# Kernel optimization log

Hardware: AMD Instinct MI355X
Metric: run time of the kernel (lower is better)

## Reference

```python
import jax, jax.numpy as jnp
import numpy as np

N_CIRC, N_MIR, N_DIS = 100_000, 50_000, 25_000
IN_CH, HID, OUT = 128, 64, 64


def setup_inputs() -> dict:
    key = jax.random.key(0)
    ks = iter(jax.random.split(key, 64))

    def nrm(shape, scale):
        return jax.random.normal(next(ks), shape, jnp.float32) * scale

    def edges(n_src, n_dst, E):
        s = jax.random.randint(next(ks), (E,), 0, n_src, jnp.int32)
        d = jax.random.randint(next(ks), (E,), 0, n_dst, jnp.int32)
        return jnp.stack([s, d])  # [2, E]

    inp = dict(
        x_circ=nrm((N_CIRC, IN_CH), 1.0),
        x_mir=nrm((N_MIR, IN_CH), 1.0),
        x_dis=nrm((N_DIS, IN_CH), 1.0),
        e_cm=edges(N_CIRC, N_MIR, 500_000),
        e_md=edges(N_MIR, N_DIS, 250_000),
        e_cd=edges(N_CIRC, N_DIS, 250_000),
        e_mc=edges(N_MIR, N_CIRC, 500_000),
        e_dm=edges(N_DIS, N_MIR, 250_000),
        e_dc=edges(N_DIS, N_CIRC, 250_000),
        e_cc=edges(N_CIRC, N_CIRC, 500_000),
        e_mm=edges(N_MIR, N_MIR, 250_000),
        # stacked SAGEConv params: lin_l (with bias) and lin_r (no bias), per relation
        W1l=nrm((6, HID, IN_CH), 0.08), W1r=nrm((6, HID, IN_CH), 0.08), b1=jnp.zeros((6, HID), jnp.float32),
        W2l=nrm((6, HID, HID), 0.12), W2r=nrm((6, HID, HID), 0.12), b2=jnp.zeros((6, HID), jnp.float32),
        W3l=nrm((8, OUT, HID), 0.12), W3r=nrm((8, OUT, HID), 0.12), b3=jnp.zeros((8, OUT), jnp.float32),
    )
    return inp


def _sage(x_src, x_dst, ei, Wl, bl, Wr, n_dst):
    # PyG SAGEConv: out = lin_l(mean_j x_src[j]) + lin_r(x_dst); isolated dst -> 0 agg
    src, dst = ei[0], ei[1]
    msum = jax.ops.segment_sum(x_src[src], dst, num_segments=n_dst)
    cnt = jax.ops.segment_sum(jnp.ones(src.shape, x_src.dtype), dst, num_segments=n_dst)
    agg = msum / jnp.maximum(cnt, 1.0)[:, None]
    return agg @ Wl.T + bl + x_dst @ Wr.T


def _hetero_layer(xc, xm, xd, Wl, Wr, b, es, with_sim):
    e_cm, e_md, e_cd, e_mc, e_dm, e_dc, e_cc, e_mm = es
    o_cm = _sage(xc, xm, e_cm, Wl[0], b[0], Wr[0], N_MIR)
    o_md = _sage(xm, xd, e_md, Wl[1], b[1], Wr[1], N_DIS)
    o_cd = _sage(xc, xd, e_cd, Wl[2], b[2], Wr[2], N_DIS)
    o_mc = _sage(xm, xc, e_mc, Wl[3], b[3], Wr[3], N_CIRC)
    o_dm = _sage(xd, xm, e_dm, Wl[4], b[4], Wr[4], N_MIR)
    o_dc = _sage(xd, xc, e_dc, Wl[5], b[5], Wr[5], N_CIRC)
    if with_sim:
        o_cc = _sage(xc, xc, e_cc, Wl[6], b[6], Wr[6], N_CIRC)
        o_mm = _sage(xm, xm, e_mm, Wl[7], b[7], Wr[7], N_MIR)
        hc = (o_mc + o_dc + o_cc) / 3.0
        hm = (o_cm + o_dm + o_mm) / 3.0
    else:
        hc = (o_mc + o_dc) / 2.0
        hm = (o_cm + o_dm) / 2.0
    hd = (o_md + o_cd) / 2.0  # HeteroConv aggr='mean' across relations
    return hc, hm, hd


def _l2norm(x):
    n = jnp.sqrt(jnp.sum(x * x, axis=1, keepdims=True))
    return x / jnp.maximum(n, 1e-12)


def reference(x_circ, x_mir, x_dis, e_cm, e_md, e_cd, e_mc, e_dm, e_dc, e_cc, e_mm,
              W1l, W1r, b1, W2l, W2r, b2, W3l, W3r, b3):
    es = (e_cm, e_md, e_cd, e_mc, e_dm, e_dc, e_cc, e_mm)
    hc, hm, hd = _hetero_layer(x_circ, x_mir, x_dis, W1l, W1r, b1, es, False)
    hc, hm, hd = jax.nn.relu(hc), jax.nn.relu(hm), jax.nn.relu(hd)  # dropout = identity (eval)
    hc, hm, hd = _hetero_layer(hc, hm, hd, W2l, W2r, b2, es, False)
    hc, hm, hd = jax.nn.relu(hc), jax.nn.relu(hm), jax.nn.relu(hd)
    oc, om, od = _hetero_layer(hc, hm, hd, W3l, W3r, b3, es, True)
    return _l2norm(oc), _l2norm(om), _l2norm(od)
```

## Files before the change

### kernel.cpp

```cpp
#include <hip/hip_runtime.h>
#include <hip/hip_bf16.h>

#define DIV_UP(a,b) (((a)+(b)-1)/(b))

typedef __bf16 bf16x8 __attribute__((ext_vector_type(8)));
typedef float  f32x4  __attribute__((ext_vector_type(4)));

__global__ __launch_bounds__(256) void detect_dtype(const unsigned int* __restrict__ x,
                                                    int* __restrict__ flag) {
  __shared__ int cnt_s;
  if (threadIdx.x == 0) cnt_s = 0;
  __syncthreads();
  unsigned w = x[threadIdx.x];
  unsigned lo_exp = (w >> 7) & 0xFF;
  if (lo_exp >= 100 && lo_exp <= 140) atomicAdd(&cnt_s, 1);
  __syncthreads();
  if (threadIdx.x == 0) flag[0] = (cnt_s >= 128) ? 1 : 0;
}

template<int K>
__global__ __launch_bounds__(256) void gemm_mfma(
    const void* __restrict__ x, int xmode,
    const void* __restrict__ w, int woff, int wmode,
    const int* __restrict__ flagp, __hip_bfloat16* __restrict__ out, int n) {
  constexpr int KP = K + 8;
  __shared__ __bf16 xs[64 * KP];
  const bool xb = (xmode == 2) ? (*flagp != 0) : (xmode == 1);
  const bool wb = (wmode == 2) ? (*flagp != 0) : (wmode == 1);
  const int t = threadIdx.x;
  const int wv = t >> 6;
  const int L = t & 63;
  const int m = L & 15, q = L >> 4;
  const int row0 = blockIdx.x * 64;
  const int col = wv * 16 + m;

  bf16x8 bfr[K / 32];
  if (wb) {
    const __bf16* wh = (const __bf16*)w + woff;
#pragma unroll
    for (int ks = 0; ks < K / 32; ++ks)
      bfr[ks] = *(const bf16x8*)&wh[col * K + ks * 32 + q * 8];
  } else {
    const float* wf = (const float*)w + woff;
#pragma unroll
    for (int ks = 0; ks < K / 32; ++ks) {
      bf16x8 b;
#pragma unroll
      for (int j = 0; j < 8; ++j) b[j] = (__bf16)wf[col * K + ks * 32 + q * 8 + j];
      bfr[ks] = b;
    }
  }

  constexpr int CH = K / 8;
  if (xb) {
    const __bf16* xh = (const __bf16*)x;
    for (int idx = t; idx < 64 * CH; idx += 256) {
      int r = idx / CH, c = idx % CH;
      int gr = row0 + r; gr = (gr < n) ? gr : (n - 1);
      *(bf16x8*)&xs[r * KP + c * 8] = *(const bf16x8*)&xh[(size_t)gr * K + c * 8];
    }
  } else {
    const float* xf = (const float*)x;
    for (int idx = t; idx < 64 * CH; idx += 256) {
      int r = idx / CH, c = idx % CH;
      int gr = row0 + r; gr = (gr < n) ? gr : (n - 1);
      const float* src = &xf[(size_t)gr * K + c * 8];
      bf16x8 v;
#pragma unroll
      for (int j = 0; j < 8; ++j) v[j] = (__bf16)src[j];
      *(bf16x8*)&xs[r * KP + c * 8] = v;
    }
  }
  __syncthreads();

  f32x4 acc[4] = {};
#pragma unroll
  for (int ks = 0; ks < K / 32; ++ks) {
#pragma unroll
    for (int rt = 0; rt < 4; ++rt) {
      bf16x8 a = *(const bf16x8*)&xs[(rt * 16 + m) * KP + ks * 32 + q * 8];
      acc[rt] = __builtin_amdgcn_mfma_f32_16x16x32_bf16(a, bfr[ks], acc[rt], 0, 0, 0);
    }
  }

#pragma unroll
  for (int rt = 0; rt < 4; ++rt) {
#pragma unroll
    for (int i = 0; i < 4; ++i) {
      int gr = row0 + rt * 16 + q * 4 + i;
      if (gr < n) out[(size_t)gr * 64 + col] = __float2bfloat16(acc[rt][i]);
    }
  }
}

template<int K, int MODE>
__global__ __launch_bounds__(256) void fused_agg(
    const void* __restrict__ xdst, int xmode,
    const int* __restrict__ flagp,
    const __hip_bfloat16* __restrict__ wrsum,
    const float* __restrict__ bias,
    const int* __restrict__ col,
    const int* __restrict__ rp0, const __hip_bfloat16* __restrict__ y0,
    const int* __restrict__ rp1, const __hip_bfloat16* __restrict__ y1,
    const int* __restrict__ rp2, const __hip_bfloat16* __restrict__ y2,
    int nrel, float invR,
    void* __restrict__ outp, size_t obase, int n) {
  __shared__ float dbuf[16][68];
  const bool xb = (xmode == 2) ? (*flagp != 0) : (xmode == 1);
  const int t = threadIdx.x;
  const int wv = t >> 6, L = t & 63;
  const int m = L & 15, q = L >> 4;
  const int row0 = blockIdx.x * 16;
  const int colc = wv * 16 + m;

  const __bf16* wh = (const __bf16*)wrsum;
  bf16x8 bfr[K / 32];
#pragma unroll
  for (int ks = 0; ks < K / 32; ++ks)
    bfr[ks] = *(const bf16x8*)&wh[colc * K + ks * 32 + q * 8];

  int ar = row0 + m; ar = (ar < n) ? ar : (n - 1);
  f32x4 acc = {};
  if (xb) {
    const __bf16* xp = (const __bf16*)xdst;
#pragma unroll
    for (int ks = 0; ks < K / 32; ++ks) {
      bf16x8 a = *(const bf16x8*)&xp[(size_t)ar * K + ks * 32 + q * 8];
      acc = __builtin_amdgcn_mfma_f32_16x16x32_bf16(a, bfr[ks], acc, 0, 0, 0);
    }
  } else {
    const float* xp = (const float*)xdst;
#pragma unroll
    for (int ks = 0; ks < K / 32; ++ks) {
      bf16x8 a;
#pragma unroll
      for (int j = 0; j < 8; ++j) a[j] = (__bf16)xp[(size_t)ar * K + ks * 32 + q * 8 + j];
      acc = __builtin_amdgcn_mfma_f32_16x16x32_bf16(a, bfr[ks], acc, 0, 0, 0);
    }
  }
  float bc = bias[colc];
#pragma unroll
  for (int i = 0; i < 4; ++i) dbuf[q * 4 + i][colc] = acc[i] + bc;
  __syncthreads();

  const int* rps[3] = {rp0, rp1, rp2};
  const __hip_bfloat16* ys[3] = {y0, y1, y2};
#pragma unroll 1
  for (int rr = 0; rr < 4; ++rr) {
    int gr = row0 + wv * 4 + rr;
    if (gr >= n) continue;
    float s = dbuf[wv * 4 + rr][L];
#pragma unroll 1
    for (int j = 0; j < nrel; ++j) {
      const int* rp = rps[j];
      const __hip_bfloat16* yy = ys[j];
      int beg = rp[gr], end = rp[gr + 1];
      if (beg == end) continue;
      float g = 0.0f;
      int e = beg;
      for (; e + 4 <= end; e += 4) {
        int c0 = col[e], c1 = col[e + 1], c2 = col[e + 2], c3 = col[e + 3];
        float v0 = __bfloat162float(yy[(size_t)c0 * 64 + L]);
        float v1 = __bfloat162float(yy[(size_t)c1 * 64 + L]);
        float v2 = __bfloat162float(yy[(size_t)c2 * 64 + L]);
        float v3 = __bfloat162float(yy[(size_t)c3 * 64 + L]);
        g += v0 + v1 + v2 + v3;
      }
      for (; e < end; ++e) g += __bfloat162float(yy[(size_t)col[e] * 64 + L]);
      s += g * (1.0f / (float)(end - beg));
    }
    s *= invR;
    if (MODE == 0) {
      ((__hip_bfloat16*)outp)[obase + (size_t)gr * 64 + L] =
          __float2bfloat16(fmaxf(s, 0.0f));
    } else {
      float ss = s * s;
#pragma unroll
      for (int o = 32; o > 0; o >>= 1) ss += __shfl_xor(ss, o, 64);
      float sc = 1.0f / fmaxf(sqrtf(ss), 1e-12f);
      float r = s * sc;
      size_t idx = obase + (size_t)gr * 64 + L;
      if (*flagp) ((__hip_bfloat16*)outp)[idx] = __float2bfloat16(r);
      else        ((float*)outp)[idx] = r;
    }
  }
}

__global__ __launch_bounds__(256) void count_int(const int* __restrict__ ed,
                                                 int* __restrict__ deg, int E) {
  int i = blockIdx.x * 256 + threadIdx.x;
  if (i < E) atomicAdd(&deg[ed[i]], 1);
}

__global__ __launch_bounds__(256) void scan1(const int* __restrict__ deg,
    int* __restrict__ outp, int* __restrict__ part, int n) {
  __shared__ int tmp[256];
  int gid = blockIdx.x * 256 + threadIdx.x;
  int v = (gid < n) ? deg[gid] : 0;
  tmp[threadIdx.x] = v;
  __syncthreads();
  for (int off = 1; off < 256; off <<= 1) {
    int t = (threadIdx.x >= off) ? tmp[threadIdx.x - off] : 0;
    __syncthreads();
    tmp[threadIdx.x] += t;
    __syncthreads();
  }
  if (gid < n) outp[gid] = tmp[threadIdx.x] - v;
  if (threadIdx.x == 255) part[blockIdx.x] = tmp[255];
}

__global__ __launch_bounds__(256) void scan2(int* __restrict__ part, int P,
                                             int* __restrict__ totalout) {
  __shared__ int tmp[256];
  __shared__ int carry;
  if (threadIdx.x == 0) carry = 0;
  __syncthreads();
  for (int base0 = 0; base0 < P; base0 += 256) {
    int i = base0 + threadIdx.x;
    int v = (i < P) ? part[i] : 0;
    tmp[threadIdx.x] = v;
    __syncthreads();
    for (int off = 1; off < 256; off <<= 1) {
      int t = (threadIdx.x >= off) ? tmp[threadIdx.x - off] : 0;
      __syncthreads();
      tmp[threadIdx.x] += t;
      __syncthreads();
    }
    if (i < P) part[i] = tmp[threadIdx.x] - v + carry;
    __syncthreads();
    if (threadIdx.x == 0) carry += tmp[255];
    __syncthreads();
  }
  if (threadIdx.x == 0) *totalout = carry;
}

__global__ __launch_bounds__(256) void scan3(int* __restrict__ outp,
    const int* __restrict__ part, int n) {
  int gid = blockIdx.x * 256 + threadIdx.x;
  if (gid < n) outp[gid] += part[blockIdx.x];
}

__global__ __launch_bounds__(256) void copy_int(const int* __restrict__ src,
                                                int* __restrict__ dst, int n) {
  int i = blockIdx.x * 256 + threadIdx.x;
  if (i < n) dst[i] = src[i];
}

__global__ __launch_bounds__(256) void fill_csr(const int* __restrict__ es,
    const int* __restrict__ ed, int* __restrict__ cursor, int* __restrict__ col, int E) {
  int i = blockIdx.x * 256 + threadIdx.x;
  if (i < E) {
    int pos = atomicAdd(&cursor[ed[i]], 1);
    col[pos] = es[i];
  }
}

__global__ __launch_bounds__(256) void wsum_kernel(
    const void* __restrict__ W, int o0, int o1, int o2,
    const void* __restrict__ B, int p0, int p1, int p2,
    const int* __restrict__ flagp, __hip_bfloat16* __restrict__ wout,
    float* __restrict__ bout, int wsz) {
  const bool bf = (*flagp != 0);
  int i = blockIdx.x * 256 + threadIdx.x;
  float s = 0.0f, sb = 0.0f;
  if (bf) {
    const __hip_bfloat16* Wp = (const __hip_bfloat16*)W;
    const __hip_bfloat16* Bp = (const __hip_bfloat16*)B;
    if (i < wsz) {
      s = __bfloat162float(Wp[o0 + i]) + __bfloat162float(Wp[o1 + i]);
      if (o2 >= 0) s += __bfloat162float(Wp[o2 + i]);
    }
    if (i < 64) {
      sb = __bfloat162float(Bp[p0 + i]) + __bfloat162float(Bp[p1 + i]);
      if (p2 >= 0) sb += __bfloat162float(Bp[p2 + i]);
    }
  } else {
    const float* Wp = (const float*)W;
    const float* Bp = (const float*)B;
    if (i < wsz) {
      s = Wp[o0 + i] + Wp[o1 + i];
      if (o2 >= 0) s += Wp[o2 + i];
    }
    if (i < 64) {
      sb = Bp[p0 + i] + Bp[p1 + i];
      if (p2 >= 0) sb += Bp[p2 + i];
    }
  }
  if (i < wsz) wout[i] = __float2bfloat16(s);
  if (i < 64) bout[i] = sb;
}

extern "C" void kernel_launch(void* const* d_in, const int* in_sizes, int n_in,
                              void* d_out, int out_size, void* d_ws, size_t ws_size,
                              hipStream_t stream) {
  const int NC = 100000, NM = 50000, ND = 25000;
  const int nn[3] = {NC, NM, ND};
  const size_t toff[3] = {0, (size_t)NC * 64, (size_t)(NC + NM) * 64};
  const void* X[3] = {d_in[0], d_in[1], d_in[2]};
  const int* eptr[8]; int E[8];
  for (int r = 0; r < 8; ++r) { eptr[r] = (const int*)d_in[3 + r]; E[r] = in_sizes[3 + r] / 2; }
  const void* Wls[3] = {d_in[11], d_in[14], d_in[17]};
  const void* Wrs[3] = {d_in[12], d_in[15], d_in[18]};
  const void* Bbs[3] = {d_in[13], d_in[16], d_in[19]};

  const int src_t[8] = {0, 1, 0, 1, 2, 2, 0, 1};
  const int dst_t[8] = {1, 2, 2, 0, 1, 0, 0, 1};
  const int relT[3][3] = {{3, 5, 6}, {0, 4, 7}, {1, 2, -1}};

  int coff[8]; int cntN = 0;
  for (int r = 0; r < 8; ++r) { coff[r] = cntN; cntN += nn[dst_t[r]]; }
  int Etot = 0; for (int r = 0; r < 8; ++r) Etot += E[r];

  char* base = (char*)d_ws;
  int* flag = (int*)base; base += 16;
  __hip_bfloat16* wr[3];
  for (int t = 0; t < 3; ++t) { wr[t] = (__hip_bfloat16*)base; base += 64 * 128 * 2; }
  float* bs[3]; for (int t = 0; t < 3; ++t) { bs[t] = (float*)base; base += 64 * 4; }
  __hip_bfloat16* y = (__hip_bfloat16*)base; base += (size_t)175000 * 64 * 2;
  int* degcur = (int*)base; base += (size_t)cntN * 4;
  int* rowptr = (int*)base; base += (size_t)(cntN + 1) * 4;
  int* part = (int*)base; base += (size_t)(DIV_UP(cntN, 256) + 1) * 4;
  int* col = (int*)base; base += (size_t)Etot * 4;
  __hip_bfloat16* h2 = (__hip_bfloat16*)base; base += (size_t)175000 * 64 * 2;
  __hip_bfloat16* h1 = (__hip_bfloat16*)d_out;
  (void)n_in; (void)out_size; (void)ws_size;

  detect_dtype<<<1, 256, 0, stream>>>((const unsigned int*)d_in[0], flag);

  hipMemsetAsync(degcur, 0, (size_t)cntN * sizeof(int), stream);
  for (int r = 0; r < 8; ++r)
    count_int<<<DIV_UP(E[r], 256), 256, 0, stream>>>(eptr[r] + E[r], degcur + coff[r], E[r]);
  int nb = DIV_UP(cntN, 256);
  scan1<<<nb, 256, 0, stream>>>(degcur, rowptr, part, cntN);
  scan2<<<1, 256, 0, stream>>>(part, nb, rowptr + cntN);
  scan3<<<nb, 256, 0, stream>>>(rowptr, part, cntN);
  copy_int<<<nb, 256, 0, stream>>>(rowptr, degcur, cntN);
  for (int r = 0; r < 8; ++r)
    fill_csr<<<DIV_UP(E[r], 256), 256, 0, stream>>>(eptr[r], eptr[r] + E[r],
                                                    degcur + coff[r], col, E[r]);

  for (int layer = 0; layer < 3; ++layer) {
    const void* Wl = Wls[layer];
    const void* Wr = Wrs[layer];
    const void* Bb = Bbs[layer];
    const int K = (layer == 0) ? 128 : 64;
    const int wsz = 64 * K;
    const __hip_bfloat16* hin = (layer == 1) ? h1 : h2;

    for (int T = 0; T < 3; ++T) {
      const int nrel = (layer == 2 && T < 2) ? 3 : 2;
      const int r0 = relT[T][0], r1 = relT[T][1];
      const int r2 = (nrel == 3) ? relT[T][2] : -1;
      wsum_kernel<<<DIV_UP(wsz, 256), 256, 0, stream>>>(
          Wr, r0 * wsz, r1 * wsz, (r2 >= 0) ? r2 * wsz : -1,
          Bb, r0 * 64, r1 * 64, (r2 >= 0) ? r2 * 64 : -1,
          flag, wr[T], bs[T], wsz);
      size_t yoffs[3] = {0, 0, 0};
      size_t yoff = 0;
      for (int j = 0; j < nrel; ++j) {
        int r = relT[T][j], st = src_t[r];
        yoffs[j] = yoff;
        if (layer == 0)
          gemm_mfma<128><<<DIV_UP(nn[st], 64), 256, 0, stream>>>(
              X[st], 2, Wl, r * wsz, 2, flag, y + yoff, nn[st]);
        else
          gemm_mfma<64><<<DIV_UP(nn[st], 64), 256, 0, stream>>>(
              hin + toff[st], 1, Wl, r * wsz, 2, flag, y + yoff, nn[st]);
        yoff += (size_t)nn[st] * 64;
      }
      const int* rp0 = rowptr + coff[r0];
      const int* rp1 = rowptr + coff[r1];
      const int* rp2 = (r2 >= 0) ? rowptr + coff[r2] : rp0;
      const __hip_bfloat16* y0 = y + yoffs[0];
      const __hip_bfloat16* y1 = y + yoffs[1];
      const __hip_bfloat16* y2 = (r2 >= 0) ? y + yoffs[2] : y0;
      int grid = DIV_UP(nn[T], 16);
      if (layer == 0) {
        fused_agg<128, 0><<<grid, 256, 0, stream>>>(
            X[T], 2, flag, wr[T], bs[T], col, rp0, y0, rp1, y1, rp2, y2,
            nrel, 0.5f, h1, toff[T], nn[T]);
      } else if (layer == 1) {
        fused_agg<64, 0><<<grid, 256, 0, stream>>>(
            h1 + toff[T], 1, flag, wr[T], bs[T], col, rp0, y0, rp1, y1, rp2, y2,
            nrel, 0.5f, h2, toff[T], nn[T]);
      } else {
        float invR = (T < 2) ? (1.0f / 3.0f) : 0.5f;
        fused_agg<64, 1><<<grid, 256, 0, stream>>>(
            h2 + toff[T], 1, flag, wr[T], bs[T], col, rp0, y0, rp1, y1, rp2, y2,
            nrel, invR, d_out, toff[T], nn[T]);
      }
    }
  }
}
```

Measured before the change: 1.214 ms.

## Balance edge aggregation across waves by splitting block edge span evenly

Instead of each wave handling four fixed destination rows, the block's combined edge range per relation is split evenly among the four waves. Partial sums go into the shared row buffer via LDS atomics, and the gather loop is unrolled to eight edges to keep more loads in flight. This targets load imbalance from varying degrees and aims to raise memory-level parallelism. The cost is extra shared-memory row-pointer staging, a row search per wave, LDS atomic adds and an additional barrier.

Measured after the change: 1.402 ms. 15.5% more time.

```diff
diff --git a/kernel.cpp b/kernel.cpp
--- a/kernel.cpp
+++ b/kernel.cpp
@@ -106,6 +106,7 @@
     int nrel, float invR,
     void* __restrict__ outp, size_t obase, int n) {
   __shared__ float dbuf[16][68];
+  __shared__ int rpl_s[3][17];
   const bool xb = (xmode == 2) ? (*flagp != 0) : (xmode == 1);
   const int t = threadIdx.x;
   const int wv = t >> 6, L = t & 63;
@@ -113,6 +114,15 @@
   const int row0 = blockIdx.x * 16;
   const int colc = wv * 16 + m;
 
+  if (t < 51) {
+    int j = t / 17, k = t - j * 17;
+    if (j < nrel) {
+      const int* rp = (j == 0) ? rp0 : (j == 1) ? rp1 : rp2;
+      int gi = row0 + k; gi = (gi < n) ? gi : n;
+      rpl_s[j][k] = rp[gi];
+    }
+  }
+
   const __bf16* wh = (const __bf16*)wrsum;
   bf16x8 bfr[K / 32];
 #pragma unroll
@@ -143,33 +153,60 @@
   for (int i = 0; i < 4; ++i) dbuf[q * 4 + i][colc] = acc[i] + bc;
   __syncthreads();
 
-  const int* rps[3] = {rp0, rp1, rp2};
   const __hip_bfloat16* ys[3] = {y0, y1, y2};
 #pragma unroll 1
-  for (int rr = 0; rr < 4; ++rr) {
-    int gr = row0 + wv * 4 + rr;
-    if (gr >= n) continue;
-    float s = dbuf[wv * 4 + rr][L];
-#pragma unroll 1
-    for (int j = 0; j < nrel; ++j) {
-      const int* rp = rps[j];
-      const __hip_bfloat16* yy = ys[j];
-      int beg = rp[gr], end = rp[gr + 1];
-      if (beg == end) continue;
+  for (int j = 0; j < nrel; ++j) {
+    const __hip_bfloat16* yy = ys[j];
+    const int* rp = &rpl_s[j][0];
+    int sb = rp[0], se = rp[16];
+    int span = se - sb;
+    if (span <= 0) continue;
+    int per = (span + 3) >> 2;
+    int e = sb + wv * per;
+    int myend = e + per; myend = (myend < se) ? myend : se;
+    if (e >= myend) continue;
+    int r = 0;
+#pragma unroll
+    for (int k = 1; k < 16; ++k) r += (e >= rp[k]);
+    int nxt = rp[r + 1];
+    while (e < myend) {
+      while (e >= nxt) { ++r; nxt = rp[r + 1]; }
+      int rbeg = rp[r];
+      float idg = 1.0f / (float)(nxt - rbeg);
+      int stop = (nxt < myend) ? nxt : myend;
       float g = 0.0f;
-      int e = beg;
-      for (; e + 4 <= end; e += 4) {
+      for (; e + 8 <= stop; e += 8) {
+        int c0 = col[e],     c1 = col[e + 1], c2 = col[e + 2], c3 = col[e + 3];
+        int c4 = col[e + 4], c5 = col[e + 5], c6 = col[e + 6], c7 = col[e + 7];
+        float v0 = __bfloat162float(yy[(size_t)c0 * 64 + L]);
+        float v1 = __bfloat162float(yy[(size_t)c1 * 64 + L]);
+        float v2 = __bfloat162float(yy[(size_t)c2 * 64 + L]);
+        float v3 = __bfloat162float(yy[(size_t)c3 * 64 + L]);
+        float v4 = __bfloat162float(yy[(size_t)c4 * 64 + L]);
+        float v5 = __bfloat162float(yy[(size_t)c5 * 64 + L]);
+        float v6 = __bfloat162float(yy[(size_t)c6 * 64 + L]);
+        float v7 = __bfloat162float(yy[(size_t)c7 * 64 + L]);
+        g += ((v0 + v1) + (v2 + v3)) + ((v4 + v5) + (v6 + v7));
+      }
+      for (; e + 4 <= stop; e += 4) {
         int c0 = col[e], c1 = col[e + 1], c2 = col[e + 2], c3 = col[e + 3];
         float v0 = __bfloat162float(yy[(size_t)c0 * 64 + L]);
         float v1 = __bfloat162float(yy[(size_t)c1 * 64 + L]);
         float v2 = __bfloat162float(yy[(size_t)c2 * 64 + L]);
         float v3 = __bfloat162float(yy[(size_t)c3 * 64 + L]);
-        g += v0 + v1 + v2 + v3;
+        g += (v0 + v1) + (v2 + v3);
       }
-      for (; e < end; ++e) g += __bfloat162float(yy[(size_t)col[e] * 64 + L]);
-      s += g * (1.0f / (float)(end - beg));
-    }
-    s *= invR;
+      for (; e < stop; ++e) g += __bfloat162float(yy[(size_t)col[e] * 64 + L]);
+      atomicAdd(&dbuf[r][L], g * idg);
+    }
+  }
+  __syncthreads();
+
+#pragma unroll 1
+  for (int rr = 0; rr < 4; ++rr) {
+    int gr = row0 + wv * 4 + rr;
+    if (gr >= n) continue;
+    float s = dbuf[wv * 4 + rr][L] * invR;
     if (MODE == 0) {
       ((__hip_bfloat16*)outp)[obase + (size_t)gr * 64 + L] =
           __float2bfloat16(fmaxf(s, 0.0f));
```

## Interleave relation gathers and stage row pointers in shared memory

Applied to the files above, without the earlier changes.

The aggregation kernel now takes the relation count as a template parameter and loads each block's row-pointer ranges into shared memory once. It then walks all relations together in batches of four edges, so gathers from different relations are in flight at the same time instead of one relation after another. The goal is more memory-level parallelism in a latency-bound gather. In exchange it uses more registers, issues redundant clamped loads for short lists, and predicates work per relation.

New measurement: 1.118 ms. 7.9% less time.

```diff
diff --git a/kernel.cpp b/kernel.cpp
--- a/kernel.cpp
+++ b/kernel.cpp
@@ -93,7 +93,7 @@
   }
 }
 
-template<int K, int MODE>
+template<int K, int MODE, int NREL>
 __global__ __launch_bounds__(256) void fused_agg(
     const void* __restrict__ xdst, int xmode,
     const int* __restrict__ flagp,
@@ -103,9 +103,10 @@
     const int* __restrict__ rp0, const __hip_bfloat16* __restrict__ y0,
     const int* __restrict__ rp1, const __hip_bfloat16* __restrict__ y1,
     const int* __restrict__ rp2, const __hip_bfloat16* __restrict__ y2,
-    int nrel, float invR,
+    float invR,
     void* __restrict__ outp, size_t obase, int n) {
   __shared__ float dbuf[16][68];
+  __shared__ int rpl_s[NREL][17];
   const bool xb = (xmode == 2) ? (*flagp != 0) : (xmode == 1);
   const int t = threadIdx.x;
   const int wv = t >> 6, L = t & 63;
@@ -113,6 +114,13 @@
   const int row0 = blockIdx.x * 16;
   const int colc = wv * 16 + m;
 
+  if (t < NREL * 17) {
+    int j = t / 17, k = t - j * 17;
+    const int* rp = (j == 0) ? rp0 : (j == 1) ? rp1 : rp2;
+    int gi = row0 + k; gi = (gi < n) ? gi : n;
+    rpl_s[j][k] = rp[gi];
+  }
+
   const __bf16* wh = (const __bf16*)wrsum;
   bf16x8 bfr[K / 32];
 #pragma unroll
@@ -143,33 +151,66 @@
   for (int i = 0; i < 4; ++i) dbuf[q * 4 + i][colc] = acc[i] + bc;
   __syncthreads();
 
-  const int* rps[3] = {rp0, rp1, rp2};
   const __hip_bfloat16* ys[3] = {y0, y1, y2};
 #pragma unroll 1
   for (int rr = 0; rr < 4; ++rr) {
-    int gr = row0 + wv * 4 + rr;
+    const int lr = wv * 4 + rr;
+    const int gr = row0 + lr;
     if (gr >= n) continue;
-    float s = dbuf[wv * 4 + rr][L];
+    float s = dbuf[lr][L];
+
+    int ptr[NREL], rem[NREL];
+    float gg[NREL], idg[NREL];
+    int nb = 0;
+#pragma unroll
+    for (int j = 0; j < NREL; ++j) {
+      int b0 = rpl_s[j][lr], e0 = rpl_s[j][lr + 1];
+      int d = e0 - b0;
+      ptr[j] = b0; rem[j] = d; gg[j] = 0.0f;
+      idg[j] = (d > 0) ? (1.0f / (float)d) : 0.0f;
+      int nbj = (d + 3) >> 2;
+      nb = (nbj > nb) ? nbj : nb;
+    }
+
 #pragma unroll 1
-    for (int j = 0; j < nrel; ++j) {
-      const int* rp = rps[j];
-      const __hip_bfloat16* yy = ys[j];
-      int beg = rp[gr], end = rp[gr + 1];
-      if (beg == end) continue;
-      float g = 0.0f;
-      int e = beg;
-      for (; e + 4 <= end; e += 4) {
-        int c0 = col[e], c1 = col[e + 1], c2 = col[e + 2], c3 = col[e + 3];
-        float v0 = __bfloat162float(yy[(size_t)c0 * 64 + L]);
-        float v1 = __bfloat162float(yy[(size_t)c1 * 64 + L]);
-        float v2 = __bfloat162float(yy[(size_t)c2 * 64 + L]);
-        float v3 = __bfloat162float(yy[(size_t)c3 * 64 + L]);
-        g += v0 + v1 + v2 + v3;
+    for (int b = 0; b < nb; ++b) {
+      int cidx[NREL][4];
+#pragma unroll
+      for (int j = 0; j < NREL; ++j) {
+        if (rem[j] > 0) {
+          int last = rem[j] - 1;
+#pragma unroll
+          for (int k = 0; k < 4; ++k) {
+            int o = (k < last) ? k : last;
+            cidx[j][k] = col[ptr[j] + o];
+          }
+        }
       }
-      for (; e < end; ++e) g += __bfloat162float(yy[(size_t)col[e] * 64 + L]);
-      s += g * (1.0f / (float)(end - beg));
-    }
+      float v[NREL][4];
+#pragma unroll
+      for (int j = 0; j < NREL; ++j) {
+        if (rem[j] > 0) {
+#pragma unroll
+          for (int k = 0; k < 4; ++k)
+            v[j][k] = __bfloat162float(ys[j][(size_t)cidx[j][k] * 64 + L]);
+        }
+      }
+#pragma unroll
+      for (int j = 0; j < NREL; ++j) {
+        if (rem[j] > 0) {
+          int rj = rem[j];
+#pragma unroll
+          for (int k = 0; k < 4; ++k)
+            gg[j] += (k < rj) ? v[j][k] : 0.0f;
+          ptr[j] += 4; rem[j] -= 4;
+        }
+      }
+    }
+
+#pragma unroll
+    for (int j = 0; j < NREL; ++j) s += gg[j] * idg[j];
     s *= invR;
+
     if (MODE == 0) {
       ((__hip_bfloat16*)outp)[obase + (size_t)gr * 64 + L] =
           __float2bfloat16(fmaxf(s, 0.0f));
@@ -376,18 +417,21 @@
       const __hip_bfloat16* y2 = (r2 >= 0) ? y + yoffs[2] : y0;
       int grid = DIV_UP(nn[T], 16);
       if (layer == 0) {
-        fused_agg<128, 0><<<grid, 256, 0, stream>>>(
+        fused_agg<128, 0, 2><<<grid, 256, 0, stream>>>(
             X[T], 2, flag, wr[T], bs[T], col, rp0, y0, rp1, y1, rp2, y2,
-            nrel, 0.5f, h1, toff[T], nn[T]);
+            0.5f, h1, toff[T], nn[T]);
       } else if (layer == 1) {
-        fused_agg<64, 0><<<grid, 256, 0, stream>>>(
+        fused_agg<64, 0, 2><<<grid, 256, 0, stream>>>(
             h1 + toff[T], 1, flag, wr[T], bs[T], col, rp0, y0, rp1, y1, rp2, y2,
-            nrel, 0.5f, h2, toff[T], nn[T]);
+            0.5f, h2, toff[T], nn[T]);
+      } else if (T < 2) {
+        fused_agg<64, 1, 3><<<grid, 256, 0, stream>>>(
+            h2 + toff[T], 1, flag, wr[T], bs[T], col, rp0, y0, rp1, y1, rp2, y2,
+            1.0f / 3.0f, d_out, toff[T], nn[T]);
       } else {
-        float invR = (T < 2) ? (1.0f / 3.0f) : 0.5f;
-        fused_agg<64, 1><<<grid, 256, 0, stream>>>(
+        fused_agg<64, 1, 2><<<grid, 256, 0, stream>>>(
             h2 + toff[T], 1, flag, wr[T], bs[T], col, rp0, y0, rp1, y1, rp2, y2,
-            nrel, invR, d_out, toff[T], nn[T]);
+            0.5f, d_out, toff[T], nn[T]);
       }
     }
   }
```
